# Kernel tuning notes

Hardware: AMD Instinct MI355X
Metric: run time of the kernel (lower is better)

Reference implementation:

```python
import jax, jax.numpy as jnp
import numpy as np

VOCAB, EMB = 50000, 300
HID, FCH = 128, 64
B, T = 1024, 200


def setup_inputs() -> dict:
    key = jax.random.key(0)
    ks = jax.random.split(key, 10)
    s = 0.05
    return {
        "x": jax.random.randint(ks[0], (B, T), 0, VOCAB),
        "emb_table": jax.random.normal(ks[1], (VOCAB, EMB), jnp.float32) * s,
        "w_ih": jax.random.normal(ks[2], (4 * HID, EMB), jnp.float32) * s,
        "w_hh": jax.random.normal(ks[3], (4 * HID, HID), jnp.float32) * s,
        "b_ih": jax.random.normal(ks[4], (4 * HID,), jnp.float32) * s,
        "b_hh": jax.random.normal(ks[5], (4 * HID,), jnp.float32) * s,
        "fc1_w": jax.random.normal(ks[6], (FCH, HID), jnp.float32) * s,
        "fc1_b": jax.random.normal(ks[7], (FCH,), jnp.float32) * s,
        "fc2_w": jax.random.normal(ks[8], (1, FCH), jnp.float32) * s,
        "fc2_b": jax.random.normal(ks[9], (1,), jnp.float32) * s,
    }


def _lstm_last_h(e, w_ih, w_hh, b_ih, b_hh):
    # e: [B, T, E] -> final hidden state [B, H]
    b, t, _ = e.shape
    h_dim = w_hh.shape[1]
    # Precompute input projections for all timesteps: [T, B, 4H]
    xg = jnp.einsum('bte,ge->tbg', e, w_ih) + (b_ih + b_hh)

    def step(carry, xg_t):
        h, c = carry
        gates = xg_t + h @ w_hh.T  # [B, 4H]
        i, f, g, o = jnp.split(gates, 4, axis=-1)  # PyTorch gate order i,f,g,o
        i = jax.nn.sigmoid(i)
        f = jax.nn.sigmoid(f)
        g = jnp.tanh(g)
        o = jax.nn.sigmoid(o)
        c = f * c + i * g
        h = o * jnp.tanh(c)
        return (h, c), None

    h0 = jnp.zeros((b, h_dim), e.dtype)
    c0 = jnp.zeros((b, h_dim), e.dtype)
    (h_n, _), _ = jax.lax.scan(step, (h0, c0), xg)
    return h_n


def reference(x, emb_table, w_ih, w_hh, b_ih, b_hh, fc1_w, fc1_b, fc2_w, fc2_b):
    e = emb_table[x]  # [B, T, E]
    hn = _lstm_last_h(e, w_ih, w_hh, b_ih, b_hh)  # [B, H]
    # dropout is identity in eval mode
    h1 = jax.nn.relu(hn @ fc1_w.T + fc1_b)  # [B, FCH]
    logits = h1 @ fc2_w.T + fc2_b  # [B, 1]
    return jax.nn.sigmoid(logits)
```

## Files before the change

### kernel.cpp

```cpp
#include <hip/hip_runtime.h>
#include <hip/hip_bf16.h>
#include <stdint.h>

#define VOCAB 50000
#define EMB   300
#define EMBP  320
#define HID   128
#define NGATE 512
#define BATCH 1024
#define SEQ   200
#define ROWS  4
#define L2E   1.4426950408889634f

typedef __attribute__((ext_vector_type(8))) short short8;
typedef __attribute__((ext_vector_type(4))) float f32x4;

#define AS1 __attribute__((address_space(1)))
#define AS3 __attribute__((address_space(3)))

static __device__ __forceinline__ void gload_lds16(const void* g, void* s) {
  __builtin_amdgcn_global_load_lds((const AS1 uint32_t*)g, (AS3 uint32_t*)s, 16, 0, 0);
}

static __device__ __forceinline__ unsigned short f2bf(float f) {
  union { float f; unsigned u; } v; v.f = f;
  unsigned r = v.u + 0x7fffu + ((v.u >> 16) & 1u);
  return (unsigned short)(r >> 16);
}
static __device__ __forceinline__ float blo2f(unsigned u) {
  union { unsigned u; float f; } v; v.u = u << 16; return v.f;
}
static __device__ __forceinline__ float bhi2f(unsigned u) {
  union { unsigned u; float f; } v; v.u = u & 0xffff0000u; return v.f;
}
static __device__ __forceinline__ float sigmf(float x) {
  return __fdividef(1.0f, 1.0f + __expf(-x));
}
static __device__ __forceinline__ float sig2(float z) {
  return __builtin_amdgcn_rcpf(1.0f + __builtin_amdgcn_exp2f(-z));
}

__global__ void k_cvt_pad(const float* __restrict__ src, unsigned short* __restrict__ dst,
                          int rows, int sc, int dc, int perm, int smode) {
  int idx = blockIdx.x * blockDim.x + threadIdx.x;
  int cpr = dc >> 3;
  if (idx >= rows * cpr) return;
  int row = idx / cpr, k0 = (idx - row * cpr) * 8;
  float s = 1.0f;
  if (smode) s = ((row >> 7) == 2) ? (2.0f * L2E) : L2E;
  uint4 pack;
  unsigned short* v = (unsigned short*)&pack;
#pragma unroll
  for (int j = 0; j < 8; j++) {
    int k = k0 + j;
    v[j] = (k < sc) ? f2bf(src[(long)row * sc + k] * s) : (unsigned short)0;
  }
  int drow = perm ? ((row & 127) * 4 + (row >> 7)) : row;
  *(uint4*)(dst + (long)drow * dc + k0) = pack;
}

__global__ void k_bias(const float* __restrict__ a, const float* __restrict__ b,
                       float* __restrict__ o) {
  int i = blockIdx.x * blockDim.x + threadIdx.x;
  if (i < NGATE) {
    int g = i >> 7, hid = i & 127;
    float s = (g == 2) ? (2.0f * L2E) : L2E;
    o[hid * 4 + g] = (a[i] + b[i]) * s;
  }
}

__global__ __launch_bounds__(256) void k_xg_gemm(
    const int* __restrict__ x, const unsigned short* __restrict__ embb,
    const unsigned short* __restrict__ wihb, const float* __restrict__ biasp,
    unsigned short* __restrict__ xg) {
  __shared__ __align__(16) unsigned short Al[2][128 * 64];
  __shared__ __align__(16) unsigned short Bl[2][128 * 64];
  const int tid = threadIdx.x;
  const int lane = tid & 63;
  const int bid = blockIdx.x;
  const int xcd = bid & 7;
  const int q = bid >> 3;
  const int tile_m = xcd * 200 + (q >> 2);
  const int tile_n = q & 3;
  const int t_idx = tile_m >> 3;
  const int b0 = (tile_m & 7) * 128;
  const int n0 = tile_n * 128;

  const int r0 = tid >> 3;
  const int sg = (tid & 7) ^ (r0 & 7);
  const unsigned short* asrc[4];
  const unsigned short* bsrc[4];
#pragma unroll
  for (int i = 0; i < 4; i++) {
    const int r = r0 + i * 32;
    const long ridx = x[(b0 + r) * SEQ + t_idx];
    asrc[i] = embb + ridx * EMBP + sg * 8;
    bsrc[i] = wihb + (long)(n0 + r) * EMBP + sg * 8;
  }

  const int wid = tid >> 6;
  const int wrow = wid >> 1, wcol = wid & 1;
  const int l15 = lane & 15, lgrp = lane >> 4;
  const int swz = (l15 & 7) << 4;

  f32x4 acc[4][4];
#pragma unroll
  for (int mt = 0; mt < 4; mt++)
#pragma unroll
    for (int nt = 0; nt < 4; nt++) acc[mt][nt] = (f32x4){0.f, 0.f, 0.f, 0.f};

#define STAGE(KS, BUF)                                                         \
  {                                                                            \
    _Pragma("unroll") for (int i = 0; i < 4; i++) {                            \
      gload_lds16(asrc[i] + (KS) * 64, (char*)Al + (BUF) * 16384 + tid * 16 + i * 4096); \
      gload_lds16(bsrc[i] + (KS) * 64, (char*)Bl + (BUF) * 16384 + tid * 16 + i * 4096); \
    }                                                                          \
  }

#define COMPUTE(BUF)                                                           \
  {                                                                            \
    const char* Ar = (const char*)Al + (BUF) * 16384 + (wrow * 64) * 128;      \
    const char* Br = (const char*)Bl + (BUF) * 16384 + (wcol * 64) * 128;      \
    _Pragma("unroll") for (int kt = 0; kt < 2; kt++) {                         \
      short8 af[4], bf[4];                                                     \
      _Pragma("unroll") for (int mt = 0; mt < 4; mt++)                         \
        af[mt] = *(const short8*)(Ar + (mt * 16 + l15) * 128 + ((kt * 64 + lgrp * 16) ^ swz)); \
      _Pragma("unroll") for (int nt = 0; nt < 4; nt++)                         \
        bf[nt] = *(const short8*)(Br + (nt * 16 + l15) * 128 + ((kt * 64 + lgrp * 16) ^ swz)); \
      _Pragma("unroll") for (int mt = 0; mt < 4; mt++)                         \
        _Pragma("unroll") for (int nt = 0; nt < 4; nt++)                       \
          acc[mt][nt] = __builtin_amdgcn_mfma_f32_16x16x32_bf16(af[mt], bf[nt], acc[mt][nt], 0, 0, 0); \
    }                                                                          \
  }

  STAGE(0, 0);
  __syncthreads();
  STAGE(1, 1); COMPUTE(0); __syncthreads();
  STAGE(2, 0); COMPUTE(1); __syncthreads();
  STAGE(3, 1); COMPUTE(0); __syncthreads();
  STAGE(4, 0); COMPUTE(1); __syncthreads();
  COMPUTE(0);
#undef STAGE
#undef COMPUTE

  const int colg = n0 + wcol * 64 + l15;
  const int rsub = lgrp * 4;
  float bv[4];
#pragma unroll
  for (int nt = 0; nt < 4; nt++) bv[nt] = biasp[colg + nt * 16];

  __syncthreads();
  char* Cb = (char*)Al;
#pragma unroll
  for (int mt = 0; mt < 4; mt++)
#pragma unroll
    for (int nt = 0; nt < 4; nt++) {
      const int nh = wcol * 64 + nt * 16 + l15;
      const int slotbase = (nh >> 3);
      const int inoff = (nh & 7) * 2;
#pragma unroll
      for (int j = 0; j < 4; j++) {
        const int mh = wrow * 64 + mt * 16 + rsub + j;
        *(unsigned short*)(Cb + mh * 256 + ((slotbase ^ (mh & 7)) << 4) + inoff) =
            f2bf(acc[mt][nt][j] + bv[nt]);
      }
    }
  __syncthreads();

  const long tile_base = (long)(tile_m * 128) * NGATE + n0;
#pragma unroll
  for (int it = 0; it < 8; it++) {
    const int row = it * 16 + (tid >> 4);
    const int ch = tid & 15;
    const uint4 v = *(const uint4*)(Cb + row * 256 + ((ch ^ (row & 7)) << 4));
    *(uint4*)((char*)xg + (tile_base + (long)row * NGATE) * 2 + ch * 16) = v;
  }
}

__global__ __launch_bounds__(512, 2) void k_lstm(
    const unsigned short* __restrict__ xg, const unsigned short* __restrict__ whhp,
    float* __restrict__ hfin) {
  __shared__ __align__(16) unsigned short h_lds[2 * 4 * 128];
  __shared__ __align__(16) float scratch[8 * 256];
  const int tid = threadIdx.x;
  const int lane = tid & 63;
  const int wid = tid >> 6;
  const int b0 = blockIdx.x * ROWS;
  const int l15 = lane & 15;
  const int lgrp = lane >> 4;
  const int hid = wid * 16 + l15;

  short8 wfr[4][4];
#pragma unroll
  for (int nt = 0; nt < 4; nt++)
#pragma unroll
    for (int kt = 0; kt < 4; kt++)
      wfr[nt][kt] = *(const short8*)(whhp + (long)(wid * 64 + nt * 16 + l15) * HID + kt * 32 + lgrp * 8);

  float c_r = 0.0f, h_r = 0.0f;

  ((unsigned*)h_lds)[tid] = 0;
  __syncthreads();

  const int ar = l15 & 3;
  int rdoff[4];
#pragma unroll
  for (int kt = 0; kt < 4; kt++)
    rdoff[kt] = ar * 256 + ((kt * 64 + lgrp * 16) ^ (ar << 5));
  const int hwoff = lgrp * 256 + ((2 * hid) ^ (lgrp << 5));
  const char* lb = (const char*)h_lds;

  float* sw = scratch + wid * 256;
  int swr[4];
#pragma unroll
  for (int nt = 0; nt < 4; nt++)
    swr[nt] = l15 * 64 + (((nt * 4 + lgrp) * 4) ^ (l15 * 4));
  const int srd = lgrp * 64 + ((l15 * 4) ^ (lgrp * 4));

  const unsigned short* xbase = xg + ((long)(b0 + lgrp) * HID + hid) * 4;
  const long TSTEP = (long)BATCH * HID * 4;
  uint2 xA = *(const uint2*)xbase;
  uint2 xB = *(const uint2*)(xbase + TSTEP);
  const unsigned short* xnext = xbase + 2 * TSTEP;

#define STEP_BODY(XS, RB, WB, T)                                               \
  {                                                                            \
    const float xf0 = blo2f(XS.x), xf1 = bhi2f(XS.x);                          \
    const float xf2 = blo2f(XS.y), xf3 = bhi2f(XS.y);                          \
    if ((T) + 2 < SEQ) XS = *(const uint2*)xnext;                              \
    short8 hf[4];                                                              \
    _Pragma("unroll") for (int kt = 0; kt < 4; kt++)                           \
      hf[kt] = *(const short8*)(lb + (RB) + rdoff[kt]);                        \
    f32x4 acc[4];                                                              \
    _Pragma("unroll") for (int nt = 0; nt < 4; nt++)                           \
      acc[nt] = (f32x4){0.f, 0.f, 0.f, 0.f};                                   \
    _Pragma("unroll") for (int kt = 0; kt < 4; kt++)                           \
      _Pragma("unroll") for (int nt = 0; nt < 4; nt++)                         \
        acc[nt] = __builtin_amdgcn_mfma_f32_16x16x32_bf16(wfr[nt][kt], hf[kt], \
                                                          acc[nt], 0, 0, 0);   \
    if (l15 < 4) {                                                             \
      _Pragma("unroll") for (int nt = 0; nt < 4; nt++)                         \
        *(f32x4*)(sw + swr[nt]) = acc[nt];                                     \
    }                                                                          \
    __builtin_amdgcn_sched_barrier(0);                                         \
    const f32x4 g4 = *(const f32x4*)(sw + srd);                                \
    const float zi = g4[0] + xf0;                                              \
    const float zf = g4[1] + xf1;                                              \
    const float zg = g4[2] + xf2;                                              \
    const float zo = g4[3] + xf3;                                              \
    const float iv = sig2(zi);                                                 \
    const float fv = sig2(zf);                                                 \
    const float gv = 2.0f * sig2(zg) - 1.0f;                                   \
    const float ov = sig2(zo);                                                 \
    c_r = fv * c_r + iv * gv;                                                  \
    const float tc = 2.0f * sig2(c_r * (2.0f * L2E)) - 1.0f;                   \
    h_r = ov * tc;                                                             \
    *(unsigned short*)((char*)h_lds + (WB) + hwoff) = f2bf(h_r);               \
    asm volatile("s_waitcnt lgkmcnt(0)" ::: "memory");                         \
    __builtin_amdgcn_s_barrier();                                              \
    __builtin_amdgcn_sched_barrier(0);                                         \
  }

  for (int t = 0; t < SEQ; t += 2) {
    STEP_BODY(xA, 0, 1024, t);
    xnext += TSTEP;
    STEP_BODY(xB, 1024, 0, t + 1);
    xnext += TSTEP;
  }
#undef STEP_BODY

  hfin[(b0 + lgrp) * HID + hid] = h_r;
}

__global__ void k_head(const float* __restrict__ hfin,
                       const float* __restrict__ fc1w, const float* __restrict__ fc1b,
                       const float* __restrict__ fc2w, const float* __restrict__ fc2b,
                       float* __restrict__ out) {
  const int tid = threadIdx.x;
  const int lane = tid & 63;
  const int wid = tid >> 6;
  const int row = blockIdx.x * 4 + wid;
  const float* h = hfin + row * HID;
  const float* w = fc1w + lane * HID;
  float acc = 0.0f;
#pragma unroll
  for (int k = 0; k < HID; k += 4) {
    const f32x4 hv = *(const f32x4*)(h + k);
    const f32x4 wv = *(const f32x4*)(w + k);
    acc += hv[0] * wv[0] + hv[1] * wv[1] + hv[2] * wv[2] + hv[3] * wv[3];
  }
  const float h1 = fmaxf(acc + fc1b[lane], 0.0f);
  float v = h1 * fc2w[lane];
#pragma unroll
  for (int off = 32; off > 0; off >>= 1) v += __shfl_down(v, off, 64);
  if (lane == 0) out[row] = sigmf(v + fc2b[0]);
}

extern "C" void kernel_launch(void* const* d_in, const int* in_sizes, int n_in,
                              void* d_out, int out_size, void* d_ws, size_t ws_size,
                              hipStream_t stream) {
  const int*   x    = (const int*)d_in[0];
  const float* emb  = (const float*)d_in[1];
  const float* w_ih = (const float*)d_in[2];
  const float* w_hh = (const float*)d_in[3];
  const float* b_ih = (const float*)d_in[4];
  const float* b_hh = (const float*)d_in[5];
  const float* fc1w = (const float*)d_in[6];
  const float* fc1b = (const float*)d_in[7];
  const float* fc2w = (const float*)d_in[8];
  const float* fc2b = (const float*)d_in[9];
  float* out = (float*)d_out;
  char* ws = (char*)d_ws;

  unsigned short* embb = (unsigned short*)(ws + 0);
  unsigned short* wihb = (unsigned short*)(ws + 32000000);
  unsigned short* whhp = (unsigned short*)(ws + 32327680);
  float*          biasp= (float*)(ws + 32458752);
  float*          hfinp= (float*)(ws + 32460800);
  unsigned short* xgb  = (unsigned short*)(ws + 32985088);

  k_cvt_pad<<<dim3((VOCAB * (EMBP / 8) + 255) / 256), dim3(256), 0, stream>>>(emb, embb, VOCAB, EMB, EMBP, 0, 0);
  k_cvt_pad<<<dim3((NGATE * (EMBP / 8) + 255) / 256), dim3(256), 0, stream>>>(w_ih, wihb, NGATE, EMB, EMBP, 1, 1);
  k_cvt_pad<<<dim3((NGATE * (HID / 8) + 255) / 256), dim3(256), 0, stream>>>(w_hh, whhp, NGATE, HID, HID, 1, 1);
  k_bias<<<dim3(2), dim3(256), 0, stream>>>(b_ih, b_hh, biasp);
  k_xg_gemm<<<dim3(1600 * 4), dim3(256), 0, stream>>>(x, embb, wihb, biasp, xgb);
  k_lstm<<<dim3(BATCH / ROWS), dim3(512), 0, stream>>>(xgb, whhp, hfinp);
  k_head<<<dim3(256), dim3(256), 0, stream>>>(hfinp, fc1w, fc1b, fc2w, fc2b, out);
  (void)in_sizes; (void)n_in; (void)out_size; (void)ws_size;
}
```

Baseline: 293.8 us.

## Halve LSTM block to 4 waves, each computing 32 hidden units

The recurrent LSTM kernel now runs with 256 threads (4 waves) instead of 512. Each wave keeps twice as many W_hh fragments in registers and issues 8 MFMA tiles per k-step, so each lane updates two hidden units per step. The first MFMA now starts from a zero constant instead of a separately zeroed accumulator. Fewer waves per block means a cheaper per-step barrier and less redundant fragment loading. The cost is more registers per lane and a longer serial MFMA chain plus gate math per wave, inside a latency-bound recurrence.

```diff
diff --git a/kernel.cpp b/kernel.cpp
--- a/kernel.cpp
+++ b/kernel.cpp
@@ -177,29 +177,28 @@
   }
 }
 
-__global__ __launch_bounds__(512, 2) void k_lstm(
+__global__ __launch_bounds__(256, 1) void k_lstm(
     const unsigned short* __restrict__ xg, const unsigned short* __restrict__ whhp,
     float* __restrict__ hfin) {
   __shared__ __align__(16) unsigned short h_lds[2 * 4 * 128];
-  __shared__ __align__(16) float scratch[8 * 256];
+  __shared__ __align__(16) float scratch[4 * 512];
   const int tid = threadIdx.x;
   const int lane = tid & 63;
   const int wid = tid >> 6;
   const int b0 = blockIdx.x * ROWS;
   const int l15 = lane & 15;
   const int lgrp = lane >> 4;
-  const int hid = wid * 16 + l15;
-
-  short8 wfr[4][4];
-#pragma unroll
-  for (int nt = 0; nt < 4; nt++)
+
+  short8 wfr[8][4];
+#pragma unroll
+  for (int nt = 0; nt < 8; nt++)
 #pragma unroll
     for (int kt = 0; kt < 4; kt++)
-      wfr[nt][kt] = *(const short8*)(whhp + (long)(wid * 64 + nt * 16 + l15) * HID + kt * 32 + lgrp * 8);
-
-  float c_r = 0.0f, h_r = 0.0f;
-
-  ((unsigned*)h_lds)[tid] = 0;
+      wfr[nt][kt] = *(const short8*)(whhp + (long)(wid * 128 + nt * 16 + l15) * HID + kt * 32 + lgrp * 8);
+
+  float c_r[2] = {0.0f, 0.0f}, h_r[2] = {0.0f, 0.0f};
+
+  ((uint2*)h_lds)[tid] = make_uint2(0, 0);
   __syncthreads();
 
   const int ar = l15 & 3;
@@ -207,55 +206,78 @@
 #pragma unroll
   for (int kt = 0; kt < 4; kt++)
     rdoff[kt] = ar * 256 + ((kt * 64 + lgrp * 16) ^ (ar << 5));
-  const int hwoff = lgrp * 256 + ((2 * hid) ^ (lgrp << 5));
+  int hwoff[2];
+#pragma unroll
+  for (int e = 0; e < 2; e++) {
+    const int hid_e = wid * 32 + e * 16 + l15;
+    hwoff[e] = lgrp * 256 + ((hid_e * 2) ^ (lgrp << 5));
+  }
   const char* lb = (const char*)h_lds;
 
-  float* sw = scratch + wid * 256;
-  int swr[4];
-#pragma unroll
-  for (int nt = 0; nt < 4; nt++)
-    swr[nt] = l15 * 64 + (((nt * 4 + lgrp) * 4) ^ (l15 * 4));
-  const int srd = lgrp * 64 + ((l15 * 4) ^ (lgrp * 4));
-
-  const unsigned short* xbase = xg + ((long)(b0 + lgrp) * HID + hid) * 4;
+  float* sw = scratch + wid * 512;
+  int swr[8];
+#pragma unroll
+  for (int nt = 0; nt < 8; nt++)
+    swr[nt] = l15 * 128 + (((nt * 4 + lgrp) ^ (l15 * 8)) << 2);
+  int srd[2];
+#pragma unroll
+  for (int e = 0; e < 2; e++)
+    srd[e] = lgrp * 128 + (((e * 16 + l15) ^ (lgrp * 8)) << 2);
+
+  const unsigned short* xbase = xg + ((long)(b0 + lgrp) * HID + wid * 32 + l15) * 4;
   const long TSTEP = (long)BATCH * HID * 4;
-  uint2 xA = *(const uint2*)xbase;
-  uint2 xB = *(const uint2*)(xbase + TSTEP);
+  uint2 xA[2], xB[2];
+#pragma unroll
+  for (int e = 0; e < 2; e++) {
+    xA[e] = *(const uint2*)(xbase + e * 64);
+    xB[e] = *(const uint2*)(xbase + TSTEP + e * 64);
+  }
   const unsigned short* xnext = xbase + 2 * TSTEP;
+  const f32x4 Z4 = (f32x4){0.f, 0.f, 0.f, 0.f};
 
 #define STEP_BODY(XS, RB, WB, T)                                               \
   {                                                                            \
-    const float xf0 = blo2f(XS.x), xf1 = bhi2f(XS.x);                          \
-    const float xf2 = blo2f(XS.y), xf3 = bhi2f(XS.y);                          \
-    if ((T) + 2 < SEQ) XS = *(const uint2*)xnext;                              \
+    float xf[8];                                                               \
+    _Pragma("unroll") for (int e = 0; e < 2; e++) {                            \
+      xf[e * 4 + 0] = blo2f(XS[e].x);                                          \
+      xf[e * 4 + 1] = bhi2f(XS[e].x);                                          \
+      xf[e * 4 + 2] = blo2f(XS[e].y);                                          \
+      xf[e * 4 + 3] = bhi2f(XS[e].y);                                          \
+    }                                                                          \
+    if ((T) + 2 < SEQ) {                                                       \
+      _Pragma("unroll") for (int e = 0; e < 2; e++)                            \
+        XS[e] = *(const uint2*)(xnext + e * 64);                               \
+    }                                                                          \
     short8 hf[4];                                                              \
     _Pragma("unroll") for (int kt = 0; kt < 4; kt++)                           \
       hf[kt] = *(const short8*)(lb + (RB) + rdoff[kt]);                        \
-    f32x4 acc[4];                                                              \
-    _Pragma("unroll") for (int nt = 0; nt < 4; nt++)                           \
-      acc[nt] = (f32x4){0.f, 0.f, 0.f, 0.f};                                   \
-    _Pragma("unroll") for (int kt = 0; kt < 4; kt++)                           \
-      _Pragma("unroll") for (int nt = 0; nt < 4; nt++)                         \
+    f32x4 acc[8];                                                              \
+    _Pragma("unroll") for (int nt = 0; nt < 8; nt++)                           \
+      acc[nt] = __builtin_amdgcn_mfma_f32_16x16x32_bf16(wfr[nt][0], hf[0], Z4, 0, 0, 0); \
+    _Pragma("unroll") for (int kt = 1; kt < 4; kt++)                           \
+      _Pragma("unroll") for (int nt = 0; nt < 8; nt++)                         \
         acc[nt] = __builtin_amdgcn_mfma_f32_16x16x32_bf16(wfr[nt][kt], hf[kt], \
                                                           acc[nt], 0, 0, 0);   \
     if (l15 < 4) {                                                             \
-      _Pragma("unroll") for (int nt = 0; nt < 4; nt++)                         \
+      _Pragma("unroll") for (int nt = 0; nt < 8; nt++)                         \
         *(f32x4*)(sw + swr[nt]) = acc[nt];                                     \
     }                                                                          \
     __builtin_amdgcn_sched_barrier(0);                                         \
-    const f32x4 g4 = *(const f32x4*)(sw + srd);                                \
-    const float zi = g4[0] + xf0;                                              \
-    const float zf = g4[1] + xf1;                                              \
-    const float zg = g4[2] + xf2;                                              \
-    const float zo = g4[3] + xf3;                                              \
-    const float iv = sig2(zi);                                                 \
-    const float fv = sig2(zf);                                                 \
-    const float gv = 2.0f * sig2(zg) - 1.0f;                                   \
-    const float ov = sig2(zo);                                                 \
-    c_r = fv * c_r + iv * gv;                                                  \
-    const float tc = 2.0f * sig2(c_r * (2.0f * L2E)) - 1.0f;                   \
-    h_r = ov * tc;                                                             \
-    *(unsigned short*)((char*)h_lds + (WB) + hwoff) = f2bf(h_r);               \
+    _Pragma("unroll") for (int e = 0; e < 2; e++) {                            \
+      const f32x4 g4 = *(const f32x4*)(sw + srd[e]);                           \
+      const float zi = g4[0] + xf[e * 4 + 0];                                  \
+      const float zf = g4[1] + xf[e * 4 + 1];                                  \
+      const float zg = g4[2] + xf[e * 4 + 2];                                  \
+      const float zo = g4[3] + xf[e * 4 + 3];                                  \
+      const float iv = sig2(zi);                                               \
+      const float fv = sig2(zf);                                               \
+      const float gv = 2.0f * sig2(zg) - 1.0f;                                 \
+      const float ov = sig2(zo);                                               \
+      c_r[e] = fv * c_r[e] + iv * gv;                                          \
+      const float tc = 2.0f * sig2(c_r[e] * (2.0f * L2E)) - 1.0f;              \
+      h_r[e] = ov * tc;                                                        \
+      *(unsigned short*)((char*)h_lds + (WB) + hwoff[e]) = f2bf(h_r[e]);       \
+    }                                                                          \
     asm volatile("s_waitcnt lgkmcnt(0)" ::: "memory");                         \
     __builtin_amdgcn_s_barrier();                                              \
     __builtin_amdgcn_sched_barrier(0);                                         \
@@ -269,7 +291,9 @@
   }
 #undef STEP_BODY
 
-  hfin[(b0 + lgrp) * HID + hid] = h_r;
+#pragma unroll
+  for (int e = 0; e < 2; e++)
+    hfin[(b0 + lgrp) * HID + wid * 32 + e * 16 + l15] = h_r[e];
 }
 
 __global__ void k_head(const float* __restrict__ hfin,
@@ -324,7 +348,7 @@
   k_cvt_pad<<<dim3((NGATE * (HID / 8) + 255) / 256), dim3(256), 0, stream>>>(w_hh, whhp, NGATE, HID, HID, 1, 1);
   k_bias<<<dim3(2), dim3(256), 0, stream>>>(b_ih, b_hh, biasp);
   k_xg_gemm<<<dim3(1600 * 4), dim3(256), 0, stream>>>(x, embb, wihb, biasp, xgb);
-  k_lstm<<<dim3(BATCH / ROWS), dim3(512), 0, stream>>>(xgb, whhp, hfinp);
+  k_lstm<<<dim3(BATCH / ROWS), dim3(256), 0, stream>>>(xgb, whhp, hfinp);
   k_head<<<dim3(256), dim3(256), 0, stream>>>(hfinp, fc1w, fc1b, fc2w, fc2b, out);
   (void)in_sizes; (void)n_in; (void)out_size; (void)ws_size;
 }
```

Result: slower. 323.3 us (+10.0%).
